# Kernel optimization log

Hardware: AMD Instinct MI355X
Metric: run time of the kernel (lower is better)

## Reference

```python
import jax, jax.numpy as jnp
import numpy as np

L, B, D, H = 2048, 2, 1024, 16
DK = D // H
SCALE = DK ** -0.5


def setup_inputs() -> dict:
    key = jax.random.key(0)
    ks = jax.random.split(key, 11)
    w_std = D ** -0.5
    return {
        "query": jax.random.normal(ks[0], (L, B, D), dtype=jnp.float32),
        "key": jax.random.normal(ks[1], (L, B, D), dtype=jnp.float32),
        "value": jax.random.normal(ks[2], (L, B, D), dtype=jnp.float32),
        "WQ_w": jax.random.normal(ks[3], (D, D), dtype=jnp.float32) * w_std,
        "WQ_b": jnp.zeros((D,), dtype=jnp.float32),
        "WK_w": jax.random.normal(ks[4], (D, D), dtype=jnp.float32) * w_std,
        "WK_b": jnp.zeros((D,), dtype=jnp.float32),
        "WV_w": jax.random.normal(ks[5], (D, D), dtype=jnp.float32) * w_std,
        "WV_b": jnp.zeros((D,), dtype=jnp.float32),
        "WO_w": jax.random.normal(ks[6], (D, D), dtype=jnp.float32) * w_std,
        "WO_b": jnp.zeros((D,), dtype=jnp.float32),
    }


def reference(query, key, value, WQ_w, WQ_b, WK_w, WK_b, WV_w, WV_b, WO_w, WO_b):
    tgt_len, batch, _ = query.shape
    src_len = key.shape[0]
    # linear projections (torch Linear: x @ W^T + b)
    q = (query @ WQ_w.T + WQ_b) * SCALE            # [L, B, D]
    k = key @ WK_w.T + WK_b                        # [S, B, D]
    v = value @ WV_w.T + WV_b                      # [S, B, D]
    # split heads: [len, B, D] -> [B*H, len, DK]
    q = q.reshape(tgt_len, batch * H, DK).transpose(1, 0, 2)
    k = k.reshape(src_len, batch * H, DK).transpose(1, 0, 2)
    v = v.reshape(src_len, batch * H, DK).transpose(1, 0, 2)
    # attention scores and softmax (full [B*H, L, S] matrix, as in the original)
    scores = jnp.einsum('nld,nsd->nls', q, k)      # [B*H, L, S]
    probs = jax.nn.softmax(scores, axis=-1)
    out = jnp.einsum('nls,nsd->nld', probs, v)     # [B*H, L, DK]
    # merge heads: [B*H, L, DK] -> [L, B, D]
    out = out.transpose(1, 0, 2).reshape(tgt_len, batch, D)
    return out @ WO_w.T + WO_b
```

## Files before the change

### kernel.cpp

```cpp
#include <hip/hip_runtime.h>
#include <hip/hip_fp16.h>

#define LL 2048
#define BB 2
#define DD 1024
#define HH 16
#define DKK 64

typedef _Float16 h8 __attribute__((ext_vector_type(8)));
typedef _Float16 h4 __attribute__((ext_vector_type(4)));
typedef float f4 __attribute__((ext_vector_type(4)));
typedef float f16v __attribute__((ext_vector_type(16)));

#define BAR() do {                                              \
    asm volatile("s_waitcnt lgkmcnt(0)" ::: "memory");          \
    __builtin_amdgcn_s_barrier();                               \
    asm volatile("" ::: "memory");                              \
} while (0)

__device__ __forceinline__ void gload_lds16(const void* g, void* l) {
    __builtin_amdgcn_global_load_lds(
        (const __attribute__((address_space(1))) void*)g,
        (__attribute__((address_space(3))) void*)l, 16, 0, 0);
}

__device__ __forceinline__ unsigned pack2h(float a, float b) {
    union { _Float16 h[2]; unsigned u; } x;
    x.h[0] = (_Float16)a; x.h[1] = (_Float16)b;
    return x.u;
}

__global__ __launch_bounds__(256) void cvt_all(
    const float* __restrict__ x0, const float* __restrict__ x1,
    const float* __restrict__ x2, const float* __restrict__ w0,
    const float* __restrict__ w1, const float* __restrict__ w2,
    const float* __restrict__ w3,
    _Float16* __restrict__ y0, _Float16* __restrict__ y1,
    _Float16* __restrict__ y2, _Float16* __restrict__ z0,
    _Float16* __restrict__ z1, _Float16* __restrict__ z2,
    _Float16* __restrict__ z3)
{
    const int sel = blockIdx.y;
    if (sel >= 3 && blockIdx.x >= 512) return;
    const float* src = (sel == 0) ? x0 : (sel == 1) ? x1 : (sel == 2) ? x2
                     : (sel == 3) ? w0 : (sel == 4) ? w1 : (sel == 5) ? w2 : w3;
    _Float16* dst = (sel == 0) ? y0 : (sel == 1) ? y1 : (sel == 2) ? y2
                  : (sel == 3) ? z0 : (sel == 4) ? z1 : (sel == 5) ? z2 : z3;
    const int i = (blockIdx.x * 256 + threadIdx.x) * 8;
    f4 a = *(const f4*)(src + i);
    f4 b = *(const f4*)(src + i + 4);
    h8 o = {(_Float16)a.x, (_Float16)a.y, (_Float16)a.z, (_Float16)a.w,
            (_Float16)b.x, (_Float16)b.y, (_Float16)b.z, (_Float16)b.w};
    *(h8*)(dst + i) = o;
}

__global__ __launch_bounds__(256) void qkv_proj(
    const _Float16* __restrict__ xq, const _Float16* __restrict__ xk,
    const _Float16* __restrict__ xv,
    const _Float16* __restrict__ wq, const float* __restrict__ bq,
    const _Float16* __restrict__ wk, const float* __restrict__ bk,
    const _Float16* __restrict__ wv, const float* __restrict__ bv,
    _Float16* __restrict__ qh, _Float16* __restrict__ kh,
    _Float16* __restrict__ vth)
{
    const int mode = blockIdx.z;
    const _Float16* X    = (mode == 0) ? xq : (mode == 1) ? xk : xv;
    const _Float16* W    = (mode == 0) ? wq : (mode == 1) ? wk : wv;
    const float*    bias = (mode == 0) ? bq : (mode == 1) ? bk : bv;

    __shared__ alignas(16) _Float16 a_sm[128 * 32];
    __shared__ alignas(16) _Float16 b_sm[128 * 32];

    const int tid  = threadIdx.x;
    const int lane = tid & 63;
    const int wave = tid >> 6;
    const int wm = (wave & 1) * 64;
    const int wn = (wave >> 1) * 64;
    const int m0 = blockIdx.x * 128;
    const int n0 = blockIdx.y * 128;

    const int srow = tid >> 2;
    const int scol = (tid & 3) * 8;
    const int lds_base = wave * 512;

    f4 acc[4][4];
    #pragma unroll
    for (int i = 0; i < 4; i++)
        #pragma unroll
        for (int j = 0; j < 4; j++)
            #pragma unroll
            for (int r = 0; r < 4; r++) acc[i][j][r] = 0.f;

    const int fr = lane & 15;
    const int fk = (lane >> 4) * 8;

    for (int k0 = 0; k0 < DD; k0 += 32) {
        gload_lds16(X + (size_t)(m0 + srow) * DD + k0 + scol,       &a_sm[lds_base]);
        gload_lds16(X + (size_t)(m0 + 64 + srow) * DD + k0 + scol,  &a_sm[2048 + lds_base]);
        gload_lds16(W + (size_t)(n0 + srow) * DD + k0 + scol,       &b_sm[lds_base]);
        gload_lds16(W + (size_t)(n0 + 64 + srow) * DD + k0 + scol,  &b_sm[2048 + lds_base]);
        __syncthreads();
        h8 af[4], bfr[4];
        #pragma unroll
        for (int i = 0; i < 4; i++) af[i]  = *(const h8*)&a_sm[(wm + i * 16 + fr) * 32 + fk];
        #pragma unroll
        for (int j = 0; j < 4; j++) bfr[j] = *(const h8*)&b_sm[(wn + j * 16 + fr) * 32 + fk];
        #pragma unroll
        for (int i = 0; i < 4; i++)
            #pragma unroll
            for (int j = 0; j < 4; j++)
                acc[i][j] = __builtin_amdgcn_mfma_f32_16x16x32_f16(af[i], bfr[j], acc[i][j], 0, 0, 0);
        __syncthreads();
    }

    const int colc = lane & 15;
    const int rowb = (lane >> 4) * 4;
    #pragma unroll
    for (int i = 0; i < 4; i++) {
        #pragma unroll
        for (int j = 0; j < 4; j++) {
            const int nn = n0 + wn + j * 16 + colc;
            const float bval = bias[nn];
            #pragma unroll
            for (int reg = 0; reg < 4; reg++) {
                const int mm = m0 + wm + i * 16 + rowb + reg;
                float v = acc[i][j][reg] + bval;
                const int b = mm & 1, l = mm >> 1;
                const int h = nn >> 6, dk = nn & 63;
                const int head = b * HH + h;
                if (mode == 0) {
                    v *= 0.1803368801111243f;
                    qh[((size_t)head * LL + l) * DKK + dk] = (_Float16)v;
                } else if (mode == 1) {
                    kh[((size_t)head * LL + l) * DKK + dk] = (_Float16)v;
                } else {
                    vth[((size_t)head * DKK + dk) * LL + l] = (_Float16)v;
                }
            }
        }
    }
}

__global__ __launch_bounds__(512, 4) void attn(
    const _Float16* __restrict__ qh, const _Float16* __restrict__ kh,
    const _Float16* __restrict__ vth, _Float16* __restrict__ oh)
{
    const int rb = blockIdx.y * 16 + blockIdx.x;
    const int lb = (rb & 7) * 64 + (rb >> 3);
    const int head = lb >> 4;
    const int q0   = (lb & 15) * 128;

    const int tid = threadIdx.x, lane = tid & 63, wave = tid >> 6;
    const int qstrip = wave & 3;
    const int sh     = wave >> 2;
    const int qw = q0 + qstrip * 32;

    __shared__ alignas(16) char smem[65536];

    const int rq = lane & 31;
    const int hi = lane >> 5;
    const int kb = hi * 8;
    const unsigned key = (unsigned)(rq & 7);

    const _Float16* khead  = kh  + (size_t)head * LL * DKK;
    const _Float16* vthead = vth + (size_t)head * DKK * LL;

    const int seg0 = wave * 2;
    auto stage = [&](int s0, unsigned koff, unsigned voff) {
        #pragma unroll
        for (int t = 0; t < 2; t++) {
            const int i = (seg0 + t) * 64 + lane;
            const int r = i >> 3, p = i & 7;
            gload_lds16(khead + (size_t)(s0 + r) * DKK + ((p ^ (r & 7)) << 3),
                        smem + koff + (unsigned)(seg0 + t) * 1024u);
        }
        #pragma unroll
        for (int t = 0; t < 2; t++) {
            const int i = (seg0 + t) * 64 + lane;
            const int r = i >> 4, p = i & 15;
            gload_lds16(vthead + (size_t)r * LL + s0 + ((p ^ (r & 7)) << 3),
                        smem + voff + (unsigned)(seg0 + t) * 1024u);
        }
    };

    stage(0, 0u, 16384u);

    const _Float16* qbase = qh + ((size_t)head * LL + qw + rq) * DKK;
    h8 qa[4];
    #pragma unroll
    for (int kf = 0; kf < 4; kf++) qa[kf] = *(const h8*)(qbase + kf * 16 + kb);

    f16v o0, o1;
    #pragma unroll
    for (int r = 0; r < 16; r++) { o0[r] = 0.f; o1[r] = 0.f; }
    float lsum = 0.f;

    asm volatile("s_waitcnt vmcnt(0)" ::: "memory");
    BAR();

    for (int it = 0; it < 16; ++it) {
        const unsigned cb = (unsigned)(it & 1) * 32768u;
        const unsigned nb = (unsigned)((it + 1) & 1) * 32768u;
        if (it < 15) stage((it + 1) * 128, nb, nb + 16384u);

        const char* kc = smem + cb;
        const char* vc = smem + cb + 16384u;

        f16v sc[2];
        #pragma unroll
        for (int st2 = 0; st2 < 2; st2++) {
            const int st = sh * 2 + st2;
            #pragma unroll
            for (int r = 0; r < 16; r++) sc[st2][r] = 0.f;
            #pragma unroll
            for (int kf = 0; kf < 4; kf++) {
                h8 kf8 = *(const h8*)(kc +
                    ((((unsigned)(st * 32 + rq) << 3) +
                      (((unsigned)(kf * 2 + hi)) ^ key)) << 4));
                sc[st2] = __builtin_amdgcn_mfma_f32_32x32x16_f16(kf8, qa[kf], sc[st2], 0, 0, 0);
            }
        }

        #pragma unroll
        for (int st2 = 0; st2 < 2; st2++) {
            const int st = sh * 2 + st2;
            float p[16];
            #pragma unroll
            for (int r = 0; r < 16; r++) {
                p[r] = __builtin_amdgcn_exp2f(sc[st2][r]);
                lsum += p[r];
            }
            unsigned w0[4], w1[4];
            #pragma unroll
            for (int g = 0; g < 4; g++) {
                w0[g] = pack2h(p[4 * g],     p[4 * g + 1]);
                w1[g] = pack2h(p[4 * g + 2], p[4 * g + 3]);
            }
            #pragma unroll
            for (int j = 0; j < 2; j++) {
                unsigned x0 = w0[2 * j], y0 = w0[2 * j + 1];
                unsigned x1 = w1[2 * j], y1 = w1[2 * j + 1];
                asm("v_permlane32_swap_b32 %0, %1" : "+v"(x0), "+v"(y0));
                asm("v_permlane32_swap_b32 %0, %1" : "+v"(x1), "+v"(y1));
                union { unsigned u[4]; h8 h; } pa;
                pa.u[0] = x0; pa.u[1] = x1; pa.u[2] = y0; pa.u[3] = y1;
                h8 b0 = *(const h8*)(vc +
                    ((((unsigned)rq << 4) +
                      (((unsigned)(st * 4 + j * 2 + hi)) ^ key)) << 4));
                h8 b1 = *(const h8*)(vc +
                    ((((unsigned)(32 + rq) << 4) +
                      (((unsigned)(st * 4 + j * 2 + hi)) ^ key)) << 4));
                o0 = __builtin_amdgcn_mfma_f32_32x32x16_f16(pa.h, b0, o0, 0, 0, 0);
                o1 = __builtin_amdgcn_mfma_f32_32x32x16_f16(pa.h, b1, o1, 0, 0, 0);
            }
        }

        asm volatile("s_waitcnt vmcnt(0)" ::: "memory");
        BAR();
    }

    lsum += __shfl_xor(lsum, 32, 64);

    float* xch = (float*)smem;
    float* lsp = (float*)(smem + 40960);
    float* myx = xch + ((qstrip * 64 + lane) * 33);
    if (sh) {
        #pragma unroll
        for (int r = 0; r < 16; r++) { myx[r] = o0[r]; myx[16 + r] = o1[r]; }
        myx[32] = lsum;
    }
    BAR();
    if (!sh) {
        #pragma unroll
        for (int r = 0; r < 16; r++) { o0[r] += myx[r]; o1[r] += myx[16 + r]; }
        lsum += myx[32];
        lsp[qstrip * 32 + rq] = 1.0f / lsum;
        asm volatile("s_waitcnt lgkmcnt(0)" ::: "memory");

        const int b = head >> 4, h = head & 15;
        #pragma unroll
        for (int r = 0; r < 16; r++) {
            const int qrow = (r & 3) + 8 * (r >> 2) + 4 * hi;
            const float inv = lsp[qstrip * 32 + qrow];
            const int ql = qw + qrow;
            const size_t base = (size_t)(ql * BB + b) * DD + h * DKK;
            oh[base + rq]      = (_Float16)(o0[r] * inv);
            oh[base + 32 + rq] = (_Float16)(o1[r] * inv);
        }
    }
}

__global__ __launch_bounds__(256) void out_proj(
    const _Float16* __restrict__ oh, const _Float16* __restrict__ wo,
    const float* __restrict__ bo, float* __restrict__ out)
{
    __shared__ alignas(16) _Float16 a_sm[64 * 32];
    __shared__ alignas(16) _Float16 b_sm[128 * 32];
    const int tid = threadIdx.x, lane = tid & 63, wave = tid >> 6;
    const int wm = (wave & 1) * 32, wn = (wave >> 1) * 64;
    const int m0 = blockIdx.x * 64, n0 = blockIdx.y * 128;

    const int srow = tid >> 2;
    const int scol = (tid & 3) * 8;
    const int lds_base = wave * 512;

    f4 acc[2][4];
    #pragma unroll
    for (int i = 0; i < 2; i++)
        #pragma unroll
        for (int j = 0; j < 4; j++)
            #pragma unroll
            for (int r = 0; r < 4; r++) acc[i][j][r] = 0.f;

    const int fr = lane & 15;
    const int fk = (lane >> 4) * 8;

    for (int k0 = 0; k0 < DD; k0 += 32) {
        gload_lds16(oh + (size_t)(m0 + srow) * DD + k0 + scol,      &a_sm[lds_base]);
        gload_lds16(wo + (size_t)(n0 + srow) * DD + k0 + scol,      &b_sm[lds_base]);
        gload_lds16(wo + (size_t)(n0 + 64 + srow) * DD + k0 + scol, &b_sm[2048 + lds_base]);
        __syncthreads();
        h8 af[2], bfr[4];
        #pragma unroll
        for (int i = 0; i < 2; i++) af[i]  = *(const h8*)&a_sm[(wm + i * 16 + fr) * 32 + fk];
        #pragma unroll
        for (int j = 0; j < 4; j++) bfr[j] = *(const h8*)&b_sm[(wn + j * 16 + fr) * 32 + fk];
        #pragma unroll
        for (int i = 0; i < 2; i++)
            #pragma unroll
            for (int j = 0; j < 4; j++)
                acc[i][j] = __builtin_amdgcn_mfma_f32_16x16x32_f16(af[i], bfr[j], acc[i][j], 0, 0, 0);
        __syncthreads();
    }

    const int colc = lane & 15;
    const int rowb = (lane >> 4) * 4;
    #pragma unroll
    for (int i = 0; i < 2; i++) {
        #pragma unroll
        for (int j = 0; j < 4; j++) {
            const int nn = n0 + wn + j * 16 + colc;
            const float bval = bo[nn];
            #pragma unroll
            for (int reg = 0; reg < 4; reg++) {
                const int mm = m0 + wm + i * 16 + rowb + reg;
                out[(size_t)mm * DD + nn] = acc[i][j][reg] + bval;
            }
        }
    }
}

extern "C" void kernel_launch(void* const* d_in, const int* in_sizes, int n_in,
                              void* d_out, int out_size, void* d_ws, size_t ws_size,
                              hipStream_t stream) {
    const float* qin = (const float*)d_in[0];
    const float* kin = (const float*)d_in[1];
    const float* vin = (const float*)d_in[2];
    const float* wq  = (const float*)d_in[3];
    const float* bq  = (const float*)d_in[4];
    const float* wk  = (const float*)d_in[5];
    const float* bk  = (const float*)d_in[6];
    const float* wv  = (const float*)d_in[7];
    const float* bv  = (const float*)d_in[8];
    const float* wo  = (const float*)d_in[9];
    const float* bo  = (const float*)d_in[10];

    const size_t seg = (size_t)32 * LL * DKK;
    _Float16* qh  = (_Float16*)d_ws;
    _Float16* kh  = qh + seg;
    _Float16* vth = kh + seg;
    _Float16* oh  = vth + seg;
    _Float16* wqh = oh + seg;
    _Float16* wkh = wqh + (size_t)DD * DD;
    _Float16* wvh = wkh + (size_t)DD * DD;
    _Float16* woh = wvh + (size_t)DD * DD;
    _Float16* xqh = woh + (size_t)DD * DD;
    _Float16* xkh = xqh + seg;
    _Float16* xvh = xkh + seg;

    hipLaunchKernelGGL(cvt_all, dim3(2048, 7), dim3(256), 0, stream,
                       qin, kin, vin, wq, wk, wv, wo,
                       xqh, xkh, xvh, wqh, wkh, wvh, woh);
    hipLaunchKernelGGL(qkv_proj, dim3(32, 8, 3), dim3(256), 0, stream,
                       xqh, xkh, xvh, wqh, bq, wkh, bk, wvh, bv, qh, kh, vth);
    hipLaunchKernelGGL(attn, dim3(16, 32), dim3(512), 0, stream, qh, kh, vth, oh);
    hipLaunchKernelGGL(out_proj, dim3(64, 8), dim3(256), 0, stream, oh, woh,
                       bo, (float*)d_out);
}
```

Before: 219.0 us.

## Fuse activation fp32-to-fp16 conversion into QKV projection; add MFMA priority hints

The activation conversion pass is removed. qkv_proj now reads fp32 activations directly, converts them in registers and writes fp16 to LDS, prefetching the next K-slice into registers during compute. This drops a full write and re-read of the half-precision activations. In exchange the projection's global A loads are fp32 (twice the bytes) and go through registers rather than the direct global-to-LDS path, and since the fp32 A tile is re-read by each of the 8 column blocks, total activation traffic may not shrink. The attention kernel also gets s_setprio around its MFMA sections and splits the row-sum into two accumulators to shorten the dependency chain.

```diff
diff --git a/kernel.cpp b/kernel.cpp
--- a/kernel.cpp
+++ b/kernel.cpp
@@ -18,6 +18,8 @@
     asm volatile("" ::: "memory");                              \
 } while (0)
 
+#define VMCNT0() asm volatile("s_waitcnt vmcnt(0)" ::: "memory")
+
 __device__ __forceinline__ void gload_lds16(const void* g, void* l) {
     __builtin_amdgcn_global_load_lds(
         (const __attribute__((address_space(1))) void*)g,
@@ -30,22 +32,15 @@
     return x.u;
 }
 
-__global__ __launch_bounds__(256) void cvt_all(
-    const float* __restrict__ x0, const float* __restrict__ x1,
-    const float* __restrict__ x2, const float* __restrict__ w0,
-    const float* __restrict__ w1, const float* __restrict__ w2,
-    const float* __restrict__ w3,
-    _Float16* __restrict__ y0, _Float16* __restrict__ y1,
-    _Float16* __restrict__ y2, _Float16* __restrict__ z0,
-    _Float16* __restrict__ z1, _Float16* __restrict__ z2,
-    _Float16* __restrict__ z3)
+__global__ __launch_bounds__(256) void cvt_w(
+    const float* __restrict__ w0, const float* __restrict__ w1,
+    const float* __restrict__ w2, const float* __restrict__ w3,
+    _Float16* __restrict__ z0, _Float16* __restrict__ z1,
+    _Float16* __restrict__ z2, _Float16* __restrict__ z3)
 {
     const int sel = blockIdx.y;
-    if (sel >= 3 && blockIdx.x >= 512) return;
-    const float* src = (sel == 0) ? x0 : (sel == 1) ? x1 : (sel == 2) ? x2
-                     : (sel == 3) ? w0 : (sel == 4) ? w1 : (sel == 5) ? w2 : w3;
-    _Float16* dst = (sel == 0) ? y0 : (sel == 1) ? y1 : (sel == 2) ? y2
-                  : (sel == 3) ? z0 : (sel == 4) ? z1 : (sel == 5) ? z2 : z3;
+    const float* src = (sel == 0) ? w0 : (sel == 1) ? w1 : (sel == 2) ? w2 : w3;
+    _Float16* dst = (sel == 0) ? z0 : (sel == 1) ? z1 : (sel == 2) ? z2 : z3;
     const int i = (blockIdx.x * 256 + threadIdx.x) * 8;
     f4 a = *(const f4*)(src + i);
     f4 b = *(const f4*)(src + i + 4);
@@ -55,8 +50,8 @@
 }
 
 __global__ __launch_bounds__(256) void qkv_proj(
-    const _Float16* __restrict__ xq, const _Float16* __restrict__ xk,
-    const _Float16* __restrict__ xv,
+    const float* __restrict__ xq, const float* __restrict__ xk,
+    const float* __restrict__ xv,
     const _Float16* __restrict__ wq, const float* __restrict__ bq,
     const _Float16* __restrict__ wk, const float* __restrict__ bk,
     const _Float16* __restrict__ wv, const float* __restrict__ bv,
@@ -64,7 +59,7 @@
     _Float16* __restrict__ vth)
 {
     const int mode = blockIdx.z;
-    const _Float16* X    = (mode == 0) ? xq : (mode == 1) ? xk : xv;
+    const float*    X    = (mode == 0) ? xq : (mode == 1) ? xk : xv;
     const _Float16* W    = (mode == 0) ? wq : (mode == 1) ? wk : wv;
     const float*    bias = (mode == 0) ? bq : (mode == 1) ? bk : bv;
 
@@ -94,12 +89,32 @@
     const int fr = lane & 15;
     const int fk = (lane >> 4) * 8;
 
+    const float* ap0 = X + (size_t)(m0 + srow) * DD + scol;
+    const float* ap1 = X + (size_t)(m0 + 64 + srow) * DD + scol;
+
+    f4 ar0 = *(const f4*)(ap0);
+    f4 ar1 = *(const f4*)(ap0 + 4);
+    f4 ar2 = *(const f4*)(ap1);
+    f4 ar3 = *(const f4*)(ap1 + 4);
+
     for (int k0 = 0; k0 < DD; k0 += 32) {
-        gload_lds16(X + (size_t)(m0 + srow) * DD + k0 + scol,       &a_sm[lds_base]);
-        gload_lds16(X + (size_t)(m0 + 64 + srow) * DD + k0 + scol,  &a_sm[2048 + lds_base]);
         gload_lds16(W + (size_t)(n0 + srow) * DD + k0 + scol,       &b_sm[lds_base]);
         gload_lds16(W + (size_t)(n0 + 64 + srow) * DD + k0 + scol,  &b_sm[2048 + lds_base]);
+        h8 a0 = {(_Float16)ar0.x, (_Float16)ar0.y, (_Float16)ar0.z, (_Float16)ar0.w,
+                 (_Float16)ar1.x, (_Float16)ar1.y, (_Float16)ar1.z, (_Float16)ar1.w};
+        h8 a1 = {(_Float16)ar2.x, (_Float16)ar2.y, (_Float16)ar2.z, (_Float16)ar2.w,
+                 (_Float16)ar3.x, (_Float16)ar3.y, (_Float16)ar3.z, (_Float16)ar3.w};
+        *(h8*)&a_sm[tid * 8]        = a0;
+        *(h8*)&a_sm[2048 + tid * 8] = a1;
         __syncthreads();
+
+        if (k0 + 32 < DD) {
+            ar0 = *(const f4*)(ap0 + k0 + 32);
+            ar1 = *(const f4*)(ap0 + k0 + 36);
+            ar2 = *(const f4*)(ap1 + k0 + 32);
+            ar3 = *(const f4*)(ap1 + k0 + 36);
+        }
+
         h8 af[4], bfr[4];
         #pragma unroll
         for (int i = 0; i < 4; i++) af[i]  = *(const h8*)&a_sm[(wm + i * 16 + fr) * 32 + fk];
@@ -193,9 +208,9 @@
     f16v o0, o1;
     #pragma unroll
     for (int r = 0; r < 16; r++) { o0[r] = 0.f; o1[r] = 0.f; }
-    float lsum = 0.f;
-
-    asm volatile("s_waitcnt vmcnt(0)" ::: "memory");
+    float lsum0 = 0.f, lsum1 = 0.f;
+
+    VMCNT0();
     BAR();
 
     for (int it = 0; it < 16; ++it) {
@@ -207,6 +222,7 @@
         const char* vc = smem + cb + 16384u;
 
         f16v sc[2];
+        __builtin_amdgcn_s_setprio(1);
         #pragma unroll
         for (int st2 = 0; st2 < 2; st2++) {
             const int st = sh * 2 + st2;
@@ -220,6 +236,7 @@
                 sc[st2] = __builtin_amdgcn_mfma_f32_32x32x16_f16(kf8, qa[kf], sc[st2], 0, 0, 0);
             }
         }
+        __builtin_amdgcn_s_setprio(0);
 
         #pragma unroll
         for (int st2 = 0; st2 < 2; st2++) {
@@ -228,7 +245,7 @@
             #pragma unroll
             for (int r = 0; r < 16; r++) {
                 p[r] = __builtin_amdgcn_exp2f(sc[st2][r]);
-                lsum += p[r];
+                if (r & 1) lsum1 += p[r]; else lsum0 += p[r];
             }
             unsigned w0[4], w1[4];
             #pragma unroll
@@ -236,6 +253,7 @@
                 w0[g] = pack2h(p[4 * g],     p[4 * g + 1]);
                 w1[g] = pack2h(p[4 * g + 2], p[4 * g + 3]);
             }
+            __builtin_amdgcn_s_setprio(1);
             #pragma unroll
             for (int j = 0; j < 2; j++) {
                 unsigned x0 = w0[2 * j], y0 = w0[2 * j + 1];
@@ -253,12 +271,14 @@
                 o0 = __builtin_amdgcn_mfma_f32_32x32x16_f16(pa.h, b0, o0, 0, 0, 0);
                 o1 = __builtin_amdgcn_mfma_f32_32x32x16_f16(pa.h, b1, o1, 0, 0, 0);
             }
-        }
-
-        asm volatile("s_waitcnt vmcnt(0)" ::: "memory");
+            __builtin_amdgcn_s_setprio(0);
+        }
+
+        VMCNT0();
         BAR();
     }
 
+    float lsum = lsum0 + lsum1;
     lsum += __shfl_xor(lsum, 32, 64);
 
     float* xch = (float*)smem;
@@ -374,15 +394,11 @@
     _Float16* wkh = wqh + (size_t)DD * DD;
     _Float16* wvh = wkh + (size_t)DD * DD;
     _Float16* woh = wvh + (size_t)DD * DD;
-    _Float16* xqh = woh + (size_t)DD * DD;
-    _Float16* xkh = xqh + seg;
-    _Float16* xvh = xkh + seg;
-
-    hipLaunchKernelGGL(cvt_all, dim3(2048, 7), dim3(256), 0, stream,
-                       qin, kin, vin, wq, wk, wv, wo,
-                       xqh, xkh, xvh, wqh, wkh, wvh, woh);
+
+    hipLaunchKernelGGL(cvt_w, dim3(512, 4), dim3(256), 0, stream,
+                       wq, wk, wv, wo, wqh, wkh, wvh, woh);
     hipLaunchKernelGGL(qkv_proj, dim3(32, 8, 3), dim3(256), 0, stream,
-                       xqh, xkh, xvh, wqh, bq, wkh, bk, wvh, bv, qh, kh, vth);
+                       qin, kin, vin, wqh, bq, wkh, bk, wvh, bv, qh, kh, vth);
     hipLaunchKernelGGL(attn, dim3(16, 32), dim3(512), 0, stream, qh, kh, vth, oh);
     hipLaunchKernelGGL(out_proj, dim3(64, 8), dim3(256), 0, stream, oh, woh,
                        bo, (float*)d_out);
```

New measurement: 226.4 us. +3.4%, slower.

## Rewrite QKV projection GEMM with 256x256 tiles, double-buffered swizzled LDS and setprio

Applied to the files above, without the earlier changes.

The QKV projection GEMM now uses 512-thread blocks with 256x256 output tiles and a K-step of 64. The K tiles are double-buffered in 128KB of XOR-swizzled LDS, and loads for the next tile are issued between MFMA quadrants so memory traffic overlaps compute. s_setprio is raised around the MFMA groups in both the GEMM and the attention kernel, and the attention row-sum is split into two accumulators to shorten its dependency chain. The larger tile cuts global reloads per FLOP, but the grid shrinks to 192 blocks, which risks leaving CUs underused, and the extra barriers add synchronisation cost.

```diff
diff --git a/kernel.cpp b/kernel.cpp
--- a/kernel.cpp
+++ b/kernel.cpp
@@ -8,7 +8,6 @@
 #define DKK 64
 
 typedef _Float16 h8 __attribute__((ext_vector_type(8)));
-typedef _Float16 h4 __attribute__((ext_vector_type(4)));
 typedef float f4 __attribute__((ext_vector_type(4)));
 typedef float f16v __attribute__((ext_vector_type(16)));
 
@@ -17,6 +16,14 @@
     __builtin_amdgcn_s_barrier();                               \
     asm volatile("" ::: "memory");                              \
 } while (0)
+
+#define SBAR() do {                                             \
+    asm volatile("" ::: "memory");                              \
+    __builtin_amdgcn_s_barrier();                               \
+    asm volatile("" ::: "memory");                              \
+} while (0)
+
+#define VMCNT0() asm volatile("s_waitcnt vmcnt(0)" ::: "memory")
 
 __device__ __forceinline__ void gload_lds16(const void* g, void* l) {
     __builtin_amdgcn_global_load_lds(
@@ -54,7 +61,7 @@
     *(h8*)(dst + i) = o;
 }
 
-__global__ __launch_bounds__(256) void qkv_proj(
+__global__ __launch_bounds__(512, 2) void qkv_proj(
     const _Float16* __restrict__ xq, const _Float16* __restrict__ xk,
     const _Float16* __restrict__ xv,
     const _Float16* __restrict__ wq, const float* __restrict__ bq,
@@ -68,62 +75,153 @@
     const _Float16* W    = (mode == 0) ? wq : (mode == 1) ? wk : wv;
     const float*    bias = (mode == 0) ? bq : (mode == 1) ? bk : bv;
 
-    __shared__ alignas(16) _Float16 a_sm[128 * 32];
-    __shared__ alignas(16) _Float16 b_sm[128 * 32];
+    __shared__ alignas(16) char smem[131072];
 
     const int tid  = threadIdx.x;
     const int lane = tid & 63;
     const int wave = tid >> 6;
-    const int wm = (wave & 1) * 64;
-    const int wn = (wave >> 1) * 64;
-    const int m0 = blockIdx.x * 128;
-    const int n0 = blockIdx.y * 128;
-
-    const int srow = tid >> 2;
-    const int scol = (tid & 3) * 8;
-    const int lds_base = wave * 512;
-
-    f4 acc[4][4];
-    #pragma unroll
-    for (int i = 0; i < 4; i++)
+    const int wm2 = wave >> 2;
+    const int wn4 = wave & 3;
+    const int m0 = blockIdx.y * 256;
+    const int n0 = blockIdx.x * 256;
+
+    const int fr = lane & 15;
+    const int g  = lane >> 4;
+
+    auto stageA = [&](int kt, int h) {
+        const unsigned base = (unsigned)((kt & 1) * 65536) + (unsigned)h * 16384u;
+        #pragma unroll
+        for (int j = 0; j < 2; j++) {
+            const int i = j * 512 + tid;
+            const int r = i >> 3, p = i & 7;
+            gload_lds16(X + (size_t)(m0 + h * 128 + r) * DD + kt * 64 + ((p ^ (r & 7)) << 3),
+                        smem + base + (unsigned)j * 8192u + (unsigned)wave * 1024u);
+        }
+    };
+    auto stageB = [&](int kt, int h) {
+        const unsigned base = (unsigned)((kt & 1) * 65536) + 32768u + (unsigned)h * 16384u;
+        #pragma unroll
+        for (int j = 0; j < 2; j++) {
+            const int i = j * 512 + tid;
+            const int r = i >> 3, p = i & 7;
+            gload_lds16(W + (size_t)(n0 + h * 128 + r) * DD + kt * 64 + ((p ^ (r & 7)) << 3),
+                        smem + base + (unsigned)j * 8192u + (unsigned)wave * 1024u);
+        }
+    };
+
+    f4 acc[8][4];
+    #pragma unroll
+    for (int i = 0; i < 8; i++)
         #pragma unroll
         for (int j = 0; j < 4; j++)
             #pragma unroll
             for (int r = 0; r < 4; r++) acc[i][j][r] = 0.f;
 
-    const int fr = lane & 15;
-    const int fk = (lane >> 4) * 8;
-
-    for (int k0 = 0; k0 < DD; k0 += 32) {
-        gload_lds16(X + (size_t)(m0 + srow) * DD + k0 + scol,       &a_sm[lds_base]);
-        gload_lds16(X + (size_t)(m0 + 64 + srow) * DD + k0 + scol,  &a_sm[2048 + lds_base]);
-        gload_lds16(W + (size_t)(n0 + srow) * DD + k0 + scol,       &b_sm[lds_base]);
-        gload_lds16(W + (size_t)(n0 + 64 + srow) * DD + k0 + scol,  &b_sm[2048 + lds_base]);
-        __syncthreads();
-        h8 af[4], bfr[4];
-        #pragma unroll
-        for (int i = 0; i < 4; i++) af[i]  = *(const h8*)&a_sm[(wm + i * 16 + fr) * 32 + fk];
-        #pragma unroll
-        for (int j = 0; j < 4; j++) bfr[j] = *(const h8*)&b_sm[(wn + j * 16 + fr) * 32 + fk];
+    auto ldA = [&](const char* bufA, int mi, int ks) -> h8 {
+        const int R = wm2 * 128 + mi * 16 + fr;
+        const int c = ks * 4 + g;
+        return *(const h8*)(bufA + (unsigned)R * 128u + (unsigned)((c ^ (R & 7)) << 4));
+    };
+    auto ldB = [&](const char* bufB, int nj, int ks) -> h8 {
+        const int R = wn4 * 64 + nj * 16 + fr;
+        const int c = ks * 4 + g;
+        return *(const h8*)(bufB + (unsigned)R * 128u + (unsigned)((c ^ (R & 7)) << 4));
+    };
+
+    stageA(0, 0); stageA(0, 1); stageB(0, 0); stageB(0, 1);
+    VMCNT0();
+    SBAR();
+
+    for (int kt = 0; kt < 16; ++kt) {
+        const char* bufA = smem + (kt & 1) * 65536;
+        const char* bufB = bufA + 32768;
+        const bool more = (kt < 15);
+
+        h8 af[4][2], bf[2][2];
+
         #pragma unroll
         for (int i = 0; i < 4; i++)
             #pragma unroll
-            for (int j = 0; j < 4; j++)
-                acc[i][j] = __builtin_amdgcn_mfma_f32_16x16x32_f16(af[i], bfr[j], acc[i][j], 0, 0, 0);
-        __syncthreads();
+            for (int ks = 0; ks < 2; ks++) af[i][ks] = ldA(bufA, i, ks);
+        #pragma unroll
+        for (int j = 0; j < 2; j++)
+            #pragma unroll
+            for (int ks = 0; ks < 2; ks++) bf[j][ks] = ldB(bufB, j, ks);
+        if (more) { stageA(kt + 1, 0); stageA(kt + 1, 1); }
+        SBAR();
+        __builtin_amdgcn_s_setprio(1);
+        #pragma unroll
+        for (int ks = 0; ks < 2; ks++)
+            #pragma unroll
+            for (int i = 0; i < 4; i++)
+                #pragma unroll
+                for (int j = 0; j < 2; j++)
+                    acc[i][j] = __builtin_amdgcn_mfma_f32_16x16x32_f16(af[i][ks], bf[j][ks], acc[i][j], 0, 0, 0);
+        __builtin_amdgcn_s_setprio(0);
+        SBAR();
+
+        #pragma unroll
+        for (int j = 0; j < 2; j++)
+            #pragma unroll
+            for (int ks = 0; ks < 2; ks++) bf[j][ks] = ldB(bufB, 2 + j, ks);
+        if (more) { stageB(kt + 1, 0); stageB(kt + 1, 1); }
+        SBAR();
+        __builtin_amdgcn_s_setprio(1);
+        #pragma unroll
+        for (int ks = 0; ks < 2; ks++)
+            #pragma unroll
+            for (int i = 0; i < 4; i++)
+                #pragma unroll
+                for (int j = 0; j < 2; j++)
+                    acc[i][2 + j] = __builtin_amdgcn_mfma_f32_16x16x32_f16(af[i][ks], bf[j][ks], acc[i][2 + j], 0, 0, 0);
+        __builtin_amdgcn_s_setprio(0);
+        SBAR();
+
+        #pragma unroll
+        for (int i = 0; i < 4; i++)
+            #pragma unroll
+            for (int ks = 0; ks < 2; ks++) af[i][ks] = ldA(bufA, 4 + i, ks);
+        SBAR();
+        __builtin_amdgcn_s_setprio(1);
+        #pragma unroll
+        for (int ks = 0; ks < 2; ks++)
+            #pragma unroll
+            for (int i = 0; i < 4; i++)
+                #pragma unroll
+                for (int j = 0; j < 2; j++)
+                    acc[4 + i][2 + j] = __builtin_amdgcn_mfma_f32_16x16x32_f16(af[i][ks], bf[j][ks], acc[4 + i][2 + j], 0, 0, 0);
+        __builtin_amdgcn_s_setprio(0);
+        SBAR();
+
+        #pragma unroll
+        for (int j = 0; j < 2; j++)
+            #pragma unroll
+            for (int ks = 0; ks < 2; ks++) bf[j][ks] = ldB(bufB, j, ks);
+        SBAR();
+        __builtin_amdgcn_s_setprio(1);
+        #pragma unroll
+        for (int ks = 0; ks < 2; ks++)
+            #pragma unroll
+            for (int i = 0; i < 4; i++)
+                #pragma unroll
+                for (int j = 0; j < 2; j++)
+                    acc[4 + i][j] = __builtin_amdgcn_mfma_f32_16x16x32_f16(af[i][ks], bf[j][ks], acc[4 + i][j], 0, 0, 0);
+        __builtin_amdgcn_s_setprio(0);
+        VMCNT0();
+        SBAR();
     }
 
     const int colc = lane & 15;
     const int rowb = (lane >> 4) * 4;
     #pragma unroll
-    for (int i = 0; i < 4; i++) {
+    for (int i = 0; i < 8; i++) {
         #pragma unroll
         for (int j = 0; j < 4; j++) {
-            const int nn = n0 + wn + j * 16 + colc;
+            const int nn = n0 + wn4 * 64 + j * 16 + colc;
             const float bval = bias[nn];
             #pragma unroll
             for (int reg = 0; reg < 4; reg++) {
-                const int mm = m0 + wm + i * 16 + rowb + reg;
+                const int mm = m0 + wm2 * 128 + i * 16 + rowb + reg;
                 float v = acc[i][j][reg] + bval;
                 const int b = mm & 1, l = mm >> 1;
                 const int h = nn >> 6, dk = nn & 63;
@@ -193,9 +291,9 @@
     f16v o0, o1;
     #pragma unroll
     for (int r = 0; r < 16; r++) { o0[r] = 0.f; o1[r] = 0.f; }
-    float lsum = 0.f;
-
-    asm volatile("s_waitcnt vmcnt(0)" ::: "memory");
+    float lsum0 = 0.f, lsum1 = 0.f;
+
+    VMCNT0();
     BAR();
 
     for (int it = 0; it < 16; ++it) {
@@ -207,6 +305,7 @@
         const char* vc = smem + cb + 16384u;
 
         f16v sc[2];
+        __builtin_amdgcn_s_setprio(1);
         #pragma unroll
         for (int st2 = 0; st2 < 2; st2++) {
             const int st = sh * 2 + st2;
@@ -220,6 +319,7 @@
                 sc[st2] = __builtin_amdgcn_mfma_f32_32x32x16_f16(kf8, qa[kf], sc[st2], 0, 0, 0);
             }
         }
+        __builtin_amdgcn_s_setprio(0);
 
         #pragma unroll
         for (int st2 = 0; st2 < 2; st2++) {
@@ -228,7 +328,7 @@
             #pragma unroll
             for (int r = 0; r < 16; r++) {
                 p[r] = __builtin_amdgcn_exp2f(sc[st2][r]);
-                lsum += p[r];
+                if (r & 1) lsum1 += p[r]; else lsum0 += p[r];
             }
             unsigned w0[4], w1[4];
             #pragma unroll
@@ -236,6 +336,7 @@
                 w0[g] = pack2h(p[4 * g],     p[4 * g + 1]);
                 w1[g] = pack2h(p[4 * g + 2], p[4 * g + 3]);
             }
+            __builtin_amdgcn_s_setprio(1);
             #pragma unroll
             for (int j = 0; j < 2; j++) {
                 unsigned x0 = w0[2 * j], y0 = w0[2 * j + 1];
@@ -253,12 +354,14 @@
                 o0 = __builtin_amdgcn_mfma_f32_32x32x16_f16(pa.h, b0, o0, 0, 0, 0);
                 o1 = __builtin_amdgcn_mfma_f32_32x32x16_f16(pa.h, b1, o1, 0, 0, 0);
             }
-        }
-
-        asm volatile("s_waitcnt vmcnt(0)" ::: "memory");
+            __builtin_amdgcn_s_setprio(0);
+        }
+
+        VMCNT0();
         BAR();
     }
 
+    float lsum = lsum0 + lsum1;
     lsum += __shfl_xor(lsum, 32, 64);
 
     float* xch = (float*)smem;
@@ -381,7 +484,7 @@
     hipLaunchKernelGGL(cvt_all, dim3(2048, 7), dim3(256), 0, stream,
                        qin, kin, vin, wq, wk, wv, wo,
                        xqh, xkh, xvh, wqh, wkh, wvh, woh);
-    hipLaunchKernelGGL(qkv_proj, dim3(32, 8, 3), dim3(256), 0, stream,
+    hipLaunchKernelGGL(qkv_proj, dim3(4, 16, 3), dim3(512), 0, stream,
                        xqh, xkh, xvh, wqh, bq, wkh, bk, wvh, bv, qh, kh, vth);
     hipLaunchKernelGGL(attn, dim3(16, 32), dim3(512), 0, stream, qh, kh, vth, oh);
     hipLaunchKernelGGL(out_proj, dim3(64, 8), dim3(256), 0, stream, oh, woh,
```

Measured after the change: 239.8 us. +9.5%, slower.

## Halve attention KV tile to 64 keys, shrink LDS, add MFMA priority hints

Applied to the files above, without the earlier changes.

The attention kernel now stages 64-key K/V tiles per iteration instead of 128, running 32 iterations, and drops LDS from 64 KB to about 34 KB. Each half-wave group processes one 32-key subtile instead of two, which lowers register pressure and lets more blocks fit per CU. It also wraps the MFMA sections in s_setprio hints and splits the row-sum accumulator into two chains. The cost is twice as many barriers and load waits per key sweep.

```diff
diff --git a/kernel.cpp b/kernel.cpp
--- a/kernel.cpp
+++ b/kernel.cpp
@@ -8,7 +8,6 @@
 #define DKK 64
 
 typedef _Float16 h8 __attribute__((ext_vector_type(8)));
-typedef _Float16 h4 __attribute__((ext_vector_type(4)));
 typedef float f4 __attribute__((ext_vector_type(4)));
 typedef float f16v __attribute__((ext_vector_type(16)));
 
@@ -17,6 +16,8 @@
     __builtin_amdgcn_s_barrier();                               \
     asm volatile("" ::: "memory");                              \
 } while (0)
+
+#define VMCNT0() asm volatile("s_waitcnt vmcnt(0)" ::: "memory")
 
 __device__ __forceinline__ void gload_lds16(const void* g, void* l) {
     __builtin_amdgcn_global_load_lds(
@@ -155,7 +156,7 @@
     const int sh     = wave >> 2;
     const int qw = q0 + qstrip * 32;
 
-    __shared__ alignas(16) char smem[65536];
+    __shared__ alignas(16) char smem[34816];
 
     const int rq = lane & 31;
     const int hi = lane >> 5;
@@ -165,25 +166,16 @@
     const _Float16* khead  = kh  + (size_t)head * LL * DKK;
     const _Float16* vthead = vth + (size_t)head * DKK * LL;
 
-    const int seg0 = wave * 2;
-    auto stage = [&](int s0, unsigned koff, unsigned voff) {
-        #pragma unroll
-        for (int t = 0; t < 2; t++) {
-            const int i = (seg0 + t) * 64 + lane;
-            const int r = i >> 3, p = i & 7;
-            gload_lds16(khead + (size_t)(s0 + r) * DKK + ((p ^ (r & 7)) << 3),
-                        smem + koff + (unsigned)(seg0 + t) * 1024u);
-        }
-        #pragma unroll
-        for (int t = 0; t < 2; t++) {
-            const int i = (seg0 + t) * 64 + lane;
-            const int r = i >> 4, p = i & 15;
-            gload_lds16(vthead + (size_t)r * LL + s0 + ((p ^ (r & 7)) << 3),
-                        smem + voff + (unsigned)(seg0 + t) * 1024u);
-        }
+    const int sr = tid >> 3, sp = tid & 7;
+    const int sgc = (sp ^ (sr & 7)) << 3;
+    auto stage = [&](int s0, unsigned base) {
+        gload_lds16(khead + (size_t)(s0 + sr) * DKK + sgc,
+                    smem + base + (unsigned)wave * 1024u);
+        gload_lds16(vthead + (size_t)sr * LL + s0 + sgc,
+                    smem + base + 8192u + (unsigned)wave * 1024u);
     };
 
-    stage(0, 0u, 16384u);
+    stage(0, 0u);
 
     const _Float16* qbase = qh + ((size_t)head * LL + qw + rq) * DKK;
     h8 qa[4];
@@ -193,76 +185,70 @@
     f16v o0, o1;
     #pragma unroll
     for (int r = 0; r < 16; r++) { o0[r] = 0.f; o1[r] = 0.f; }
-    float lsum = 0.f;
-
-    asm volatile("s_waitcnt vmcnt(0)" ::: "memory");
+    float lsum0 = 0.f, lsum1 = 0.f;
+
+    VMCNT0();
     BAR();
 
-    for (int it = 0; it < 16; ++it) {
-        const unsigned cb = (unsigned)(it & 1) * 32768u;
-        const unsigned nb = (unsigned)((it + 1) & 1) * 32768u;
-        if (it < 15) stage((it + 1) * 128, nb, nb + 16384u);
+    for (int it = 0; it < 32; ++it) {
+        const unsigned cb = (unsigned)(it & 1) * 16384u;
+        const unsigned nb = cb ^ 16384u;
+        if (it < 31) stage((it + 1) * 64, nb);
 
         const char* kc = smem + cb;
-        const char* vc = smem + cb + 16384u;
-
-        f16v sc[2];
-        #pragma unroll
-        for (int st2 = 0; st2 < 2; st2++) {
-            const int st = sh * 2 + st2;
-            #pragma unroll
-            for (int r = 0; r < 16; r++) sc[st2][r] = 0.f;
-            #pragma unroll
-            for (int kf = 0; kf < 4; kf++) {
-                h8 kf8 = *(const h8*)(kc +
-                    ((((unsigned)(st * 32 + rq) << 3) +
-                      (((unsigned)(kf * 2 + hi)) ^ key)) << 4));
-                sc[st2] = __builtin_amdgcn_mfma_f32_32x32x16_f16(kf8, qa[kf], sc[st2], 0, 0, 0);
-            }
-        }
-
-        #pragma unroll
-        for (int st2 = 0; st2 < 2; st2++) {
-            const int st = sh * 2 + st2;
-            float p[16];
-            #pragma unroll
-            for (int r = 0; r < 16; r++) {
-                p[r] = __builtin_amdgcn_exp2f(sc[st2][r]);
-                lsum += p[r];
-            }
-            unsigned w0[4], w1[4];
-            #pragma unroll
-            for (int g = 0; g < 4; g++) {
-                w0[g] = pack2h(p[4 * g],     p[4 * g + 1]);
-                w1[g] = pack2h(p[4 * g + 2], p[4 * g + 3]);
-            }
-            #pragma unroll
-            for (int j = 0; j < 2; j++) {
-                unsigned x0 = w0[2 * j], y0 = w0[2 * j + 1];
-                unsigned x1 = w1[2 * j], y1 = w1[2 * j + 1];
-                asm("v_permlane32_swap_b32 %0, %1" : "+v"(x0), "+v"(y0));
-                asm("v_permlane32_swap_b32 %0, %1" : "+v"(x1), "+v"(y1));
-                union { unsigned u[4]; h8 h; } pa;
-                pa.u[0] = x0; pa.u[1] = x1; pa.u[2] = y0; pa.u[3] = y1;
-                h8 b0 = *(const h8*)(vc +
-                    ((((unsigned)rq << 4) +
-                      (((unsigned)(st * 4 + j * 2 + hi)) ^ key)) << 4));
-                h8 b1 = *(const h8*)(vc +
-                    ((((unsigned)(32 + rq) << 4) +
-                      (((unsigned)(st * 4 + j * 2 + hi)) ^ key)) << 4));
-                o0 = __builtin_amdgcn_mfma_f32_32x32x16_f16(pa.h, b0, o0, 0, 0, 0);
-                o1 = __builtin_amdgcn_mfma_f32_32x32x16_f16(pa.h, b1, o1, 0, 0, 0);
-            }
-        }
-
-        asm volatile("s_waitcnt vmcnt(0)" ::: "memory");
+        const char* vc = smem + cb + 8192u;
+
+        f16v sc;
+        #pragma unroll
+        for (int r = 0; r < 16; r++) sc[r] = 0.f;
+        __builtin_amdgcn_s_setprio(1);
+        #pragma unroll
+        for (int kf = 0; kf < 4; kf++) {
+            h8 kf8 = *(const h8*)(kc +
+                ((((unsigned)(sh * 32 + rq) << 3) +
+                  (((unsigned)(kf * 2 + hi)) ^ key)) << 4));
+            sc = __builtin_amdgcn_mfma_f32_32x32x16_f16(kf8, qa[kf], sc, 0, 0, 0);
+        }
+        __builtin_amdgcn_s_setprio(0);
+
+        float p[16];
+        #pragma unroll
+        for (int r = 0; r < 16; r++) {
+            p[r] = __builtin_amdgcn_exp2f(sc[r]);
+            if (r & 1) lsum1 += p[r]; else lsum0 += p[r];
+        }
+        unsigned w0[4], w1[4];
+        #pragma unroll
+        for (int g = 0; g < 4; g++) {
+            w0[g] = pack2h(p[4 * g],     p[4 * g + 1]);
+            w1[g] = pack2h(p[4 * g + 2], p[4 * g + 3]);
+        }
+        __builtin_amdgcn_s_setprio(1);
+        #pragma unroll
+        for (int j = 0; j < 2; j++) {
+            unsigned x0 = w0[2 * j], y0 = w0[2 * j + 1];
+            unsigned x1 = w1[2 * j], y1 = w1[2 * j + 1];
+            asm("v_permlane32_swap_b32 %0, %1" : "+v"(x0), "+v"(y0));
+            asm("v_permlane32_swap_b32 %0, %1" : "+v"(x1), "+v"(y1));
+            union { unsigned u[4]; h8 h; } pa;
+            pa.u[0] = x0; pa.u[1] = x1; pa.u[2] = y0; pa.u[3] = y1;
+            const unsigned c = ((unsigned)(sh * 4 + j * 2 + hi)) ^ key;
+            h8 b0 = *(const h8*)(vc + ((((unsigned)rq << 3) + c) << 4));
+            h8 b1 = *(const h8*)(vc + ((((unsigned)(32 + rq) << 3) + c) << 4));
+            o0 = __builtin_amdgcn_mfma_f32_32x32x16_f16(pa.h, b0, o0, 0, 0, 0);
+            o1 = __builtin_amdgcn_mfma_f32_32x32x16_f16(pa.h, b1, o1, 0, 0, 0);
+        }
+        __builtin_amdgcn_s_setprio(0);
+
+        VMCNT0();
         BAR();
     }
 
+    float lsum = lsum0 + lsum1;
     lsum += __shfl_xor(lsum, 32, 64);
 
     float* xch = (float*)smem;
-    float* lsp = (float*)(smem + 40960);
+    float* lsp = (float*)(smem + 33792);
     float* myx = xch + ((qstrip * 64 + lane) * 33);
     if (sh) {
         #pragma unroll
```

After: 222.6 us. No clear change (+1.7%).
